# Optimization experiments

Measured on AMD Instinct MI355X. Metric: run time of the kernel, lower is better.

## Reference

```python
import jax, jax.numpy as jnp
import numpy as np

B, T, V, D, U, NT = 32, 512, 32000, 300, 300, 3


def setup_inputs() -> dict:
    key = jax.random.key(0)
    ks = jax.random.split(key, 10)
    s = 0.05
    return {
        "inputs": jax.random.randint(ks[0], (B, T), 0, V),
        "sequence_length": jax.random.randint(ks[1], (B,), 0, T),
        "emb": jax.random.normal(ks[2], (V, D), jnp.float32) * s,
        "Wk_f": jax.random.normal(ks[3], (D, 4 * U), jnp.float32) * s,
        "Wr_f": jax.random.normal(ks[4], (U, 4 * U), jnp.float32) * s,
        "b_f": jnp.zeros((4 * U,), jnp.float32),
        "Wk_b": jax.random.normal(ks[5], (D, 4 * U), jnp.float32) * s,
        "Wr_b": jax.random.normal(ks[6], (U, 4 * U), jnp.float32) * s,
        "b_b": jnp.zeros((4 * U,), jnp.float32),
        "fc_W": jax.random.normal(ks[7], (2 * U, NT), jnp.float32) * s,
        "fc_b": jnp.zeros((NT,), jnp.float32),
    }


def _lstm_scan(x, mask, Wk, Wr, b):
    # x: [B,T,D], mask: [B,T] bool. Keras semantics: masked steps carry h,c through.
    units = Wr.shape[0]
    zx = jnp.einsum('btd,dz->btz', x, Wk) + b        # precompute input projection
    zx_t = jnp.swapaxes(zx, 0, 1)                    # [T,B,4U]
    m_t = jnp.swapaxes(mask, 0, 1)                   # [T,B]

    def step(carry, inp):
        h, c = carry
        zxt, mt = inp
        z = zxt + h @ Wr                             # [B,4U]
        i, f, g, o = jnp.split(z, 4, axis=-1)
        c_new = jax.nn.sigmoid(f) * c + jax.nn.sigmoid(i) * jnp.tanh(g)
        h_new = jax.nn.sigmoid(o) * jnp.tanh(c_new)
        m = mt[:, None]
        h = jnp.where(m, h_new, h)
        c = jnp.where(m, c_new, c)
        return (h, c), h

    h0 = jnp.zeros((x.shape[0], units), x.dtype)
    _, hs = jax.lax.scan(step, (h0, h0), (zx_t, m_t))
    return jnp.swapaxes(hs, 0, 1)                    # [B,T,U]


def reference(inputs, sequence_length, emb, Wk_f, Wr_f, b_f, Wk_b, Wr_b, b_b, fc_W, fc_b):
    x = emb[inputs]                                   # [B,T,D]
    mask = jnp.arange(T)[None, :] < sequence_length[:, None]  # [B,T]
    h_fwd = _lstm_scan(x, mask, Wk_f, Wr_f, b_f)
    # backward direction: reverse time (input + mask), scan, reverse output back
    h_bwd = jnp.flip(_lstm_scan(jnp.flip(x, 1), jnp.flip(mask, 1), Wk_b, Wr_b, b_b), 1)
    h = jnp.concatenate([h_fwd, h_bwd], axis=-1)      # [B,T,2U]
    return h @ fc_W + fc_b                            # [B,T,NT]
```

## Files before the change

### kernel.cpp

```cpp
#include <hip/hip_runtime.h>
#include <stdint.h>


#define BB 32
#define TT 512
#define DD 300
#define UU 300
#define G4 1200
#define NTOK 3

#define KB   10
#define UPB  30
#define NCOL 120
#define KTILES 10
#define HSTR 320
#define HROW 304

#define WKROWS 1280
#define WKSTR  320

typedef uint16_t bf16_t;
typedef short  s16x8 __attribute__((ext_vector_type(8)));
typedef float  f32x4 __attribute__((ext_vector_type(4)));

union U8 { unsigned long long q[2]; s16x8 v; };

__device__ __forceinline__ float bf2f(uint16_t u) {
    union { uint32_t i; float f; } v; v.i = ((uint32_t)u) << 16; return v.f;
}
__device__ __forceinline__ uint16_t f2bf(float f) {
    union { uint32_t i; float f; } v; v.f = f;
    uint32_t r = v.i + 0x7fffu + ((v.i >> 16) & 1u);
    return (uint16_t)(r >> 16);
}
__device__ __forceinline__ float ldf(const void* base, size_t idx, int f32m) {
    return f32m ? ((const float*)base)[idx]
                : bf2f(((const uint16_t*)base)[idx]);
}

__device__ __forceinline__ f32x4 xpose4(f32x4 v, int lane) {
    f32x4 t, w, s, r;
    t[0] = __shfl_xor(v[0], 1); t[1] = __shfl_xor(v[1], 1);
    t[2] = __shfl_xor(v[2], 1); t[3] = __shfl_xor(v[3], 1);
    if ((lane & 1) == 0) { w[0]=v[0]; w[1]=t[0]; w[2]=v[2]; w[3]=t[2]; }
    else                 { w[0]=t[1]; w[1]=v[1]; w[2]=t[3]; w[3]=v[3]; }
    s[0] = __shfl_xor(w[0], 2); s[1] = __shfl_xor(w[1], 2);
    s[2] = __shfl_xor(w[2], 2); s[3] = __shfl_xor(w[3], 2);
    if ((lane & 2) == 0) { r[0]=w[0]; r[1]=w[1]; r[2]=s[0]; r[3]=s[1]; }
    else                 { r[0]=s[2]; r[1]=s[3]; r[2]=w[2]; r[3]=w[3]; }
    return r;
}

__device__ __forceinline__ float fsig(float x) {
    return __builtin_amdgcn_rcpf(1.f + __expf(-x));
}
__device__ __forceinline__ float ftanh(float x) {
    float cx = fminf(10.f, fmaxf(-10.f, x));
    float e = __expf(2.f * cx);
    return (e - 1.f) * __builtin_amdgcn_rcpf(e + 1.f);
}

__device__ __forceinline__ void gatefn(f32x4 zv, uint2 zp, bool m,
                                       float& c, float& h) {
    float zi = zv[0] + bf2f((uint16_t)(zp.x & 0xffff));
    float zf = zv[1] + bf2f((uint16_t)(zp.x >> 16));
    float zg = zv[2] + bf2f((uint16_t)(zp.y & 0xffff));
    float zo = zv[3] + bf2f((uint16_t)(zp.y >> 16));
    float si = fsig(zi);
    float sf = fsig(zf);
    float so = fsig(zo);
    float tg = ftanh(zg);
    float cn = sf * c + si * tg;
    float hn = so * ftanh(cn);
    if (m) { c = cn; h = hn; }
}

__global__ void detect_dtype(const uint16_t* __restrict__ emb_u16,
                             int* __restrict__ flag) {
    __shared__ float red[256];
    const int tid = threadIdx.x;
    float m = 0.f;
    for (int k = tid; k < 4096; k += 256)
        m = fmaxf(m, fabsf(bf2f(emb_u16[2 * k])));
    red[tid] = m;
    __syncthreads();
    for (int s = 128; s > 0; s >>= 1) {
        if (tid < s) red[tid] = fmaxf(red[tid], red[tid + s]);
        __syncthreads();
    }
    if (tid == 0) flag[0] = (red[0] > 1.0e3f) ? 1 : 0;
}

__global__ void prep_wrp(const void* __restrict__ Wr_f,
                         const void* __restrict__ Wr_b,
                         bf16_t* __restrict__ WrPT_f,
                         bf16_t* __restrict__ WrPT_b,
                         const int* __restrict__ flagp) {
    const int f32m = *flagp;
    int idx = blockIdx.x * 256 + threadIdx.x;
    const void* src = blockIdx.y ? Wr_b : Wr_f;
    bf16_t*     dst = blockIdx.y ? WrPT_b : WrPT_f;
    if (idx < G4 * HROW) {
        int p = idx / HROW;
        int k = idx - p * HROW;
        int u = p >> 2, g = p & 3;
        float v = (k < DD) ? ldf(src, (size_t)k * G4 + g * UU + u, f32m) : 0.f;
        dst[idx] = f2bf(v);
    }
}

__global__ void prep_wkt(const void* __restrict__ Wk_f, const void* __restrict__ b_f,
                         const void* __restrict__ Wk_b, const void* __restrict__ b_b,
                         bf16_t* __restrict__ WkT, bf16_t* __restrict__ biasP,
                         const int* __restrict__ flagp) {
    const int f32m = *flagp;
    const int dir = blockIdx.y;
    const void* Wk = dir ? Wk_b : Wk_f;
    const void* bs = dir ? b_b  : b_f;
    bf16_t* dst = WkT + (size_t)dir * (WKROWS * WKSTR);
    int idx = blockIdx.x * 256 + threadIdx.x;
    if (idx < WKROWS * WKSTR) {
        int p = idx / WKSTR;
        int k = idx - p * WKSTR;
        int u = p >> 2, g = p & 3;
        float v = (p < G4 && k < DD) ? ldf(Wk, (size_t)k * G4 + g * UU + u, f32m)
                                     : 0.f;
        dst[idx] = f2bf(v);
        if (idx < WKROWS) {
            int pp = idx, uu = pp >> 2, gg = pp & 3;
            biasP[dir * WKROWS + idx] =
                (pp < G4) ? f2bf(ldf(bs, gg * UU + uu, f32m)) : (bf16_t)0;
        }
    }
}

__global__ void init_state(bf16_t* __restrict__ Hglob, int* __restrict__ flags) {
    int i = blockIdx.x * 256 + threadIdx.x;
    if (i < 2 * 2 * BB * HROW) Hglob[i] = 0;
    if (i < 2 * TT * 16) flags[i] = 0;
}

#define ZM 64
#define ZN 128
__global__ __launch_bounds__(256, 2) void zx_gemm2(
    const int* __restrict__ inputs, const void* __restrict__ emb,
    const bf16_t* __restrict__ WkTall, const bf16_t* __restrict__ biasP,
    bf16_t* __restrict__ zxf, bf16_t* __restrict__ zxb,
    const int* __restrict__ flagp) {

    const int f32m = *flagp;
    const int dir = blockIdx.z;
    const bf16_t* WkT = WkTall + (size_t)dir * (WKROWS * WKSTR);
    const bf16_t* bp  = biasP + dir * WKROWS;
    bf16_t* out = dir ? zxb : zxf;

    const int tid = threadIdx.x;
    const int pb = blockIdx.x * ZN;
    const int rowBase = blockIdx.y * ZM;

    __shared__ __align__(16) uint16_t Alds[ZM * HSTR];
    __shared__ int rowids[ZM];

    if (tid < ZM) rowids[tid] = inputs[rowBase + tid];
    for (int i = tid; i < ZM * HSTR; i += 256) Alds[i] = 0;
    __syncthreads();

    for (int i = tid; i < ZM * 38; i += 256) {
        int r = i / 38, g = i - 38 * r;
        int k0 = g * 8;
        const size_t eb = (size_t)rowids[r] * DD + k0;
        uint16_t tmp[8];
        if (g < 37) {
            if (f32m) {
                const float* ef = (const float*)emb + eb;
#pragma unroll
                for (int e = 0; e < 8; e++) tmp[e] = f2bf(ef[e]);
            } else {
                *(uint4*)tmp = *(const uint4*)((const uint16_t*)emb + eb);
            }
        } else {
#pragma unroll
            for (int e = 0; e < 8; e++) {
                int k = k0 + e;
                tmp[e] = (k < DD)
                    ? (f32m ? f2bf(((const float*)emb)[(size_t)rowids[r] * DD + k])
                            : ((const uint16_t*)emb)[(size_t)rowids[r] * DD + k])
                    : (uint16_t)0;
            }
        }
        *(uint4*)&Alds[r * HSTR + ((g ^ (r & 7)) << 3)] = *(uint4*)tmp;
    }
    __syncthreads();

    const int lane = tid & 63;
    const int wv   = tid >> 6;
    const int q    = lane >> 4;
    const int c16  = lane & 15;
    const int n0   = 32 * wv;
    const int sw7  = c16 & 7;

    f32x4 acc[4][2];
#pragma unroll
    for (int mt = 0; mt < 4; mt++)
        for (int nh = 0; nh < 2; nh++) acc[mt][nh] = (f32x4){0.f,0.f,0.f,0.f};

    const int p0 = pb + n0 + c16;
    const int p1 = p0 + 16;
#pragma unroll
    for (int kt = 0; kt < KTILES; kt++) {
        int k0 = 32 * kt + 8 * q;
        int sw = (((kt * 4 + q) ^ sw7) << 3);
        s16x8 b0 = *(const s16x8*)&WkT[(size_t)p0 * WKSTR + k0];
        s16x8 b1 = *(const s16x8*)&WkT[(size_t)p1 * WKSTR + k0];
#pragma unroll
        for (int mt = 0; mt < 4; mt++) {
            s16x8 af = *(const s16x8*)&Alds[(16 * mt + c16) * HSTR + sw];
            acc[mt][0] = __builtin_amdgcn_mfma_f32_16x16x32_bf16(af, b0, acc[mt][0], 0, 0, 0);
            acc[mt][1] = __builtin_amdgcn_mfma_f32_16x16x32_bf16(af, b1, acc[mt][1], 0, 0, 0);
        }
    }

    __syncthreads();
    float* Cs = (float*)Alds;
#pragma unroll
    for (int mt = 0; mt < 4; mt++)
#pragma unroll
        for (int nh = 0; nh < 2; nh++)
#pragma unroll
            for (int r = 0; r < 4; r++)
                Cs[(16 * mt + 4 * q + r) * 132 + n0 + 16 * nh + c16] = acc[mt][nh][r];
    __syncthreads();

    for (int i = tid; i < ZM * (ZN / 2); i += 256) {
        int r = i >> 6, cc = (i & 63) * 2;
        int p = pb + cc;
        if (p < G4) {
            float v0 = Cs[r * 132 + cc]     + bf2f(bp[p]);
            float v1 = Cs[r * 132 + cc + 1] + bf2f(bp[p + 1]);
            uint32_t pk = (uint32_t)f2bf(v0) | ((uint32_t)f2bf(v1) << 16);
            *(uint32_t*)&out[(size_t)(rowBase + r) * G4 + p] = pk;
        }
    }
}

__global__ __launch_bounds__(256, 1) void lstm_rec4(
    const bf16_t* __restrict__ zxf, const bf16_t* __restrict__ zxb,
    const bf16_t* __restrict__ WrPT_f, const bf16_t* __restrict__ WrPT_b,
    const int* __restrict__ seqlen,
    bf16_t* __restrict__ Hglob, int* __restrict__ flags,
    bf16_t* __restrict__ hf, bf16_t* __restrict__ hb) {

    const int blk = blockIdx.x % KB;
    const int dir = blockIdx.x / KB;
    const bf16_t* zx   = dir ? zxb    : zxf;
    const bf16_t* WrPT = dir ? WrPT_b : WrPT_f;
    bf16_t*       hout = dir ? hb : hf;
    bf16_t*       Hg   = Hglob + (size_t)dir * (2 * BB * HROW);
    int*          fbase = flags + dir * (TT * 16);

    __shared__ __align__(16) uint16_t Hlds[BB * HSTR];
    __shared__ uint16_t hstage[BB * UPB];

    const int tid  = threadIdx.x;
    const int lane = tid & 63;
    const int wv   = tid >> 6;
    const int q    = lane >> 4;
    const int c16  = lane & 15;
    const int n0   = 32 * wv;
    const int sw7  = c16 & 7;
    const int k4   = c16 >> 2;
    const int j4   = c16 & 3;
    const int u0   = 8 * wv + k4;
    const int b0   = 4 * q + j4;
    const bool v1  = (u0 + 4 < UPB);
    const bool pollme = (lane < KB) && (lane != blk);

    for (int i = tid; i < BB * HSTR; i += 256) Hlds[i] = 0;
    U8 Bf0[KTILES], Bf1[KTILES];
#pragma unroll
    for (int kt = 0; kt < KTILES; kt++) {
        int k0 = 32 * kt + 8 * q;
        int col0 = n0 + c16, col1 = n0 + 16 + c16;
        U8 z; z.q[0] = 0; z.q[1] = 0;
        Bf0[kt] = z; Bf1[kt] = z;
        if (k0 < 304) {
            if (col0 < NCOL)
                Bf0[kt].v = *(const s16x8*)&WrPT[(size_t)(NCOL * blk + col0) * HROW + k0];
            if (col1 < NCOL)
                Bf1[kt].v = *(const s16x8*)&WrPT[(size_t)(NCOL * blk + col1) * HROW + k0];
        }
    }
    float c00 = 0.f, c01 = 0.f, c10 = 0.f, c11 = 0.f;
    float h00 = 0.f, h01 = 0.f, h10 = 0.f, h11 = 0.f;
    const int L0 = seqlen[b0];
    const int L1 = seqlen[b0 + 16];
    __syncthreads();

    for (int ts = 0; ts < TT; ts++) {
        const int t = dir ? (TT - 1 - ts) : ts;

        const size_t zr0 = ((size_t)(b0 * TT + t)) * G4 + NCOL * blk;
        const size_t zr1 = ((size_t)((b0 + 16) * TT + t)) * G4 + NCOL * blk;
        uint2 z00 = *(const uint2*)&zx[zr0 + 4 * u0];
        uint2 z10 = *(const uint2*)&zx[zr1 + 4 * u0];
        uint2 z01 = {0, 0}, z11 = {0, 0};
        if (v1) {
            z01 = *(const uint2*)&zx[zr0 + 4 * (u0 + 4)];
            z11 = *(const uint2*)&zx[zr1 + 4 * (u0 + 4)];
        }

        if (ts > 0) {
            int* fl = fbase + (ts - 1) * 16;
            int a = pollme ? __hip_atomic_load(&fl[lane], __ATOMIC_RELAXED,
                                               __HIP_MEMORY_SCOPE_AGENT) : 1;
            if (!__all(a != 0)) {
                int b = pollme ? __hip_atomic_load(&fl[lane], __ATOMIC_RELAXED,
                                                   __HIP_MEMORY_SCOPE_AGENT) : 1;
                int c = pollme ? __hip_atomic_load(&fl[lane], __ATOMIC_RELAXED,
                                                   __HIP_MEMORY_SCOPE_AGENT) : 1;
                for (;;) {
                    if (__all(a != 0)) break;
                    a = b; b = c;
                    c = pollme ? __hip_atomic_load(&fl[lane], __ATOMIC_RELAXED,
                                                   __HIP_MEMORY_SCOPE_AGENT) : 1;
                }
            }
        }

        const unsigned long long* Hsrc64 =
            (const unsigned long long*)(Hg + (size_t)(ts & 1) * (BB * HROW));
        unsigned long long hv[10];
#pragma unroll
        for (int k = 0; k < 9; k++)
            hv[k] = __hip_atomic_load(&Hsrc64[tid + 256 * k], __ATOMIC_RELAXED,
                                      __HIP_MEMORY_SCOPE_AGENT);
        if (tid < 128)
            hv[9] = __hip_atomic_load(&Hsrc64[2304 + tid], __ATOMIC_RELAXED,
                                      __HIP_MEMORY_SCOPE_AGENT);
#pragma unroll
        for (int k = 0; k < 9; k++) {
            int i = tid + 256 * k;
            int b = i / 76, x = i - 76 * b;
            *(unsigned long long*)
                &Hlds[b * HSTR + ((((x >> 1) ^ (b & 7)) << 3) | ((x & 1) << 2))]
                = hv[k];
        }
        if (tid < 128) {
            int i = 2304 + tid;
            int b = i / 76, x = i - 76 * b;
            *(unsigned long long*)
                &Hlds[b * HSTR + ((((x >> 1) ^ (b & 7)) << 3) | ((x & 1) << 2))]
                = hv[9];
        }
        __syncthreads();

        f32x4 acc00 = {0.f,0.f,0.f,0.f}, acc01 = {0.f,0.f,0.f,0.f};
        f32x4 acc10 = {0.f,0.f,0.f,0.f}, acc11 = {0.f,0.f,0.f,0.f};
#pragma unroll
        for (int kt = 0; kt < KTILES; kt++) {
            int sw = (((kt * 4 + q) ^ sw7) << 3);
            s16x8 a0 = *(const s16x8*)&Hlds[c16 * HSTR + sw];
            s16x8 a1 = *(const s16x8*)&Hlds[(c16 + 16) * HSTR + sw];
            acc00 = __builtin_amdgcn_mfma_f32_16x16x32_bf16(a0, Bf0[kt].v, acc00, 0, 0, 0);
            acc01 = __builtin_amdgcn_mfma_f32_16x16x32_bf16(a0, Bf1[kt].v, acc01, 0, 0, 0);
            acc10 = __builtin_amdgcn_mfma_f32_16x16x32_bf16(a1, Bf0[kt].v, acc10, 0, 0, 0);
            acc11 = __builtin_amdgcn_mfma_f32_16x16x32_bf16(a1, Bf1[kt].v, acc11, 0, 0, 0);
        }

        f32x4 t00 = xpose4(acc00, lane);
        f32x4 t01 = xpose4(acc01, lane);
        f32x4 t10 = xpose4(acc10, lane);
        f32x4 t11 = xpose4(acc11, lane);
        const bool m0 = (t < L0);
        const bool m1 = (t < L1);
        gatefn(t00, z00, m0, c00, h00);
        gatefn(t01, z01, m0, c01, h01);
        gatefn(t10, z10, m1, c10, h10);
        gatefn(t11, z11, m1, c11, h11);

        hstage[b0 * UPB + u0]        = f2bf(h00);
        hstage[(b0 + 16) * UPB + u0] = f2bf(h10);
        if (v1) {
            hstage[b0 * UPB + u0 + 4]        = f2bf(h01);
            hstage[(b0 + 16) * UPB + u0 + 4] = f2bf(h11);
        }
        __syncthreads();

        if (ts < TT - 1) {
            bf16_t* Hdst = Hg + (size_t)((ts + 1) & 1) * (BB * HROW);
            for (int i = tid; i < BB * (UPB / 2); i += 256) {
                int b = i / (UPB / 2), k = i - b * (UPB / 2);
                uint32_t val = (uint32_t)hstage[b * UPB + 2 * k] |
                               ((uint32_t)hstage[b * UPB + 2 * k + 1] << 16);
                __hip_atomic_store(
                    (uint32_t*)&Hdst[b * HROW + UPB * blk + 2 * k], val,
                    __ATOMIC_RELAXED, __HIP_MEMORY_SCOPE_AGENT);
            }
            __syncthreads();
            if (tid == 0)
                __hip_atomic_store(&fbase[ts * 16 + blk], 1, __ATOMIC_RELAXED,
                                   __HIP_MEMORY_SCOPE_AGENT);
        }

        for (int i = tid; i < BB * (UPB / 2); i += 256) {
            int b = i / (UPB / 2), k = i - b * (UPB / 2);
            uint32_t val = (uint32_t)hstage[b * UPB + 2 * k] |
                           ((uint32_t)hstage[b * UPB + 2 * k + 1] << 16);
            *(uint32_t*)&hout[((size_t)(b * TT + t)) * UU + UPB * blk + 2 * k] = val;
        }
    }
}

__global__ __launch_bounds__(256) void fc_out(
    const bf16_t* __restrict__ hf, const bf16_t* __restrict__ hb,
    const void* __restrict__ fcW, const void* __restrict__ fcb,
    void* __restrict__ out, const int* __restrict__ flagp) {

    const int f32m = *flagp;
    __shared__ float W[2 * UU * NTOK];
    __shared__ float bias[NTOK];
    const int tid = threadIdx.x;
    for (int i = tid; i < 2 * UU * NTOK; i += 256) W[i] = ldf(fcW, i, f32m);
    if (tid < NTOK) bias[tid] = ldf(fcb, tid, f32m);
    __syncthreads();

    const int r = blockIdx.x * 256 + tid;
    const bf16_t* hfr = hf + (size_t)r * UU;
    const bf16_t* hbr = hb + (size_t)r * UU;
    float s0 = bias[0], s1 = bias[1], s2 = bias[2];
    for (int u = 0; u < UU; u++) {
        float f = bf2f(hfr[u]);
        s0 += f * W[u * 3 + 0];
        s1 += f * W[u * 3 + 1];
        s2 += f * W[u * 3 + 2];
    }
    for (int u = 0; u < UU; u++) {
        float f = bf2f(hbr[u]);
        s0 += f * W[(UU + u) * 3 + 0];
        s1 += f * W[(UU + u) * 3 + 1];
        s2 += f * W[(UU + u) * 3 + 2];
    }
    if (f32m) {
        float* o = (float*)out;
        o[(size_t)r * 3 + 0] = s0;
        o[(size_t)r * 3 + 1] = s1;
        o[(size_t)r * 3 + 2] = s2;
    } else {
        bf16_t* o = (bf16_t*)out;
        o[(size_t)r * 3 + 0] = f2bf(s0);
        o[(size_t)r * 3 + 1] = f2bf(s1);
        o[(size_t)r * 3 + 2] = f2bf(s2);
    }
}

extern "C" void kernel_launch(void* const* d_in, const int* in_sizes, int n_in,
                              void* d_out, int out_size, void* d_ws, size_t ws_size,
                              hipStream_t stream) {
    const int* inputs = (const int*)d_in[0];
    const int* seqlen = (const int*)d_in[1];
    const void* emb  = d_in[2];
    const void* Wk_f = d_in[3];
    const void* Wr_f = d_in[4];
    const void* b_f  = d_in[5];
    const void* Wk_b = d_in[6];
    const void* Wr_b = d_in[7];
    const void* b_b  = d_in[8];
    const void* fcW  = d_in[9];
    const void* fcb  = d_in[10];

    char* ws = (char*)d_ws;
    int*    flag   = (int*)(ws + 0);
    int*    flags  = (int*)(ws + 64);
    bf16_t* Hglob  = (bf16_t*)(ws + 65664);
    bf16_t* WrPT_f = (bf16_t*)(ws + 143488);
    bf16_t* WrPT_b = (bf16_t*)(ws + 873088);
    bf16_t* zxPf   = (bf16_t*)(ws + 1602688);
    bf16_t* zxPb   = (bf16_t*)(ws + 40924288);
    bf16_t* hfbuf  = (bf16_t*)(ws + 80245888);
    bf16_t* hbbuf  = (bf16_t*)(ws + 90076288);
    bf16_t* WkT    = hfbuf;
    bf16_t* biasP  = hfbuf + 2 * WKROWS * WKSTR;

    detect_dtype<<<1, 256, 0, stream>>>((const uint16_t*)emb, flag);
    {
        dim3 grid((G4 * HROW + 255) / 256, 2);
        prep_wrp<<<grid, 256, 0, stream>>>(Wr_f, Wr_b, WrPT_f, WrPT_b, flag);
    }
    {
        dim3 grid((WKROWS * WKSTR + 255) / 256, 2);
        prep_wkt<<<grid, 256, 0, stream>>>(Wk_f, b_f, Wk_b, b_b, WkT, biasP, flag);
    }
    init_state<<<64, 256, 0, stream>>>(Hglob, flags);
    {
        dim3 grid(10, 256, 2);
        zx_gemm2<<<grid, 256, 0, stream>>>(inputs, emb, WkT, biasP,
                                           zxPf, zxPb, flag);
    }
    lstm_rec4<<<2 * KB, 256, 0, stream>>>(zxPf, zxPb, WrPT_f, WrPT_b, seqlen,
                                          Hglob, flags, hfbuf, hbbuf);
    fc_out<<<(BB * TT) / 256, 256, 0, stream>>>(hfbuf, hbbuf, fcW, fcb,
                                                d_out, flag);
}
```

Before: 1.823 ms.

## Loop over all output column tiles per block to reuse gathered embedding rows

The input-projection GEMM now has each block gather its 64 embedding rows into LDS once and then iterate over all 10 column tiles, instead of launching 10 blocks that each re-gather the same rows. The epilogue drops the LDS staging and writes bf16 pairs straight from registers, using a lane shuffle to pack adjacent columns. This cuts redundant embedding gathers, zero-fills and barriers, but leaves only 512 blocks, fewer than before, and the direct stores are less coalesced.

```diff
diff --git a/kernel.cpp b/kernel.cpp
--- a/kernel.cpp
+++ b/kernel.cpp
@@ -142,21 +142,20 @@
 
 #define ZM 64
 #define ZN 128
-__global__ __launch_bounds__(256, 2) void zx_gemm2(
+__global__ __launch_bounds__(256, 2) void zx_gemm3(
     const int* __restrict__ inputs, const void* __restrict__ emb,
     const bf16_t* __restrict__ WkTall, const bf16_t* __restrict__ biasP,
     bf16_t* __restrict__ zxf, bf16_t* __restrict__ zxb,
     const int* __restrict__ flagp) {
 
     const int f32m = *flagp;
-    const int dir = blockIdx.z;
+    const int dir = blockIdx.y;
     const bf16_t* WkT = WkTall + (size_t)dir * (WKROWS * WKSTR);
     const bf16_t* bp  = biasP + dir * WKROWS;
     bf16_t* out = dir ? zxb : zxf;
 
     const int tid = threadIdx.x;
-    const int pb = blockIdx.x * ZN;
-    const int rowBase = blockIdx.y * ZM;
+    const int rowBase = blockIdx.x * ZM;
 
     __shared__ __align__(16) uint16_t Alds[ZM * HSTR];
     __shared__ int rowids[ZM];
@@ -198,47 +197,51 @@
     const int c16  = lane & 15;
     const int n0   = 32 * wv;
     const int sw7  = c16 & 7;
-
-    f32x4 acc[4][2];
-#pragma unroll
-    for (int mt = 0; mt < 4; mt++)
-        for (int nh = 0; nh < 2; nh++) acc[mt][nh] = (f32x4){0.f,0.f,0.f,0.f};
-
-    const int p0 = pb + n0 + c16;
-    const int p1 = p0 + 16;
-#pragma unroll
-    for (int kt = 0; kt < KTILES; kt++) {
-        int k0 = 32 * kt + 8 * q;
-        int sw = (((kt * 4 + q) ^ sw7) << 3);
-        s16x8 b0 = *(const s16x8*)&WkT[(size_t)p0 * WKSTR + k0];
-        s16x8 b1 = *(const s16x8*)&WkT[(size_t)p1 * WKSTR + k0];
+    const bool evn = ((lane & 1) == 0);
+
+    for (int nt = 0; nt < 10; nt++) {
+        const int pb = nt * ZN;
+        const int p0 = pb + n0 + c16;
+        const int p1 = p0 + 16;
+        const float bv0 = bf2f(bp[p0]);
+        const float bv1 = bf2f(bp[p1]);
+
+        f32x4 acc[4][2];
+#pragma unroll
+        for (int mt = 0; mt < 4; mt++)
+            for (int nh = 0; nh < 2; nh++) acc[mt][nh] = (f32x4){0.f,0.f,0.f,0.f};
+
+#pragma unroll
+        for (int kt = 0; kt < KTILES; kt++) {
+            int k0 = 32 * kt + 8 * q;
+            int sw = (((kt * 4 + q) ^ sw7) << 3);
+            s16x8 b0 = *(const s16x8*)&WkT[(size_t)p0 * WKSTR + k0];
+            s16x8 b1 = *(const s16x8*)&WkT[(size_t)p1 * WKSTR + k0];
+#pragma unroll
+            for (int mt = 0; mt < 4; mt++) {
+                s16x8 af = *(const s16x8*)&Alds[(16 * mt + c16) * HSTR + sw];
+                acc[mt][0] = __builtin_amdgcn_mfma_f32_16x16x32_bf16(af, b0, acc[mt][0], 0, 0, 0);
+                acc[mt][1] = __builtin_amdgcn_mfma_f32_16x16x32_bf16(af, b1, acc[mt][1], 0, 0, 0);
+            }
+        }
+
 #pragma unroll
         for (int mt = 0; mt < 4; mt++) {
-            s16x8 af = *(const s16x8*)&Alds[(16 * mt + c16) * HSTR + sw];
-            acc[mt][0] = __builtin_amdgcn_mfma_f32_16x16x32_bf16(af, b0, acc[mt][0], 0, 0, 0);
-            acc[mt][1] = __builtin_amdgcn_mfma_f32_16x16x32_bf16(af, b1, acc[mt][1], 0, 0, 0);
-        }
-    }
-
-    __syncthreads();
-    float* Cs = (float*)Alds;
-#pragma unroll
-    for (int mt = 0; mt < 4; mt++)
-#pragma unroll
-        for (int nh = 0; nh < 2; nh++)
-#pragma unroll
-            for (int r = 0; r < 4; r++)
-                Cs[(16 * mt + 4 * q + r) * 132 + n0 + 16 * nh + c16] = acc[mt][nh][r];
-    __syncthreads();
-
-    for (int i = tid; i < ZM * (ZN / 2); i += 256) {
-        int r = i >> 6, cc = (i & 63) * 2;
-        int p = pb + cc;
-        if (p < G4) {
-            float v0 = Cs[r * 132 + cc]     + bf2f(bp[p]);
-            float v1 = Cs[r * 132 + cc + 1] + bf2f(bp[p + 1]);
-            uint32_t pk = (uint32_t)f2bf(v0) | ((uint32_t)f2bf(v1) << 16);
-            *(uint32_t*)&out[(size_t)(rowBase + r) * G4 + p] = pk;
+#pragma unroll
+            for (int nh = 0; nh < 2; nh++) {
+                const int p = (nh == 0) ? p0 : p1;
+                const float bv = (nh == 0) ? bv0 : bv1;
+#pragma unroll
+                for (int r = 0; r < 4; r++) {
+                    uint32_t mine = f2bf(acc[mt][nh][r] + bv);
+                    uint32_t other = (uint32_t)__shfl_xor((int)mine, 1);
+                    if (evn && p < G4) {
+                        uint32_t pk = mine | (other << 16);
+                        int row = rowBase + 16 * mt + 4 * q + r;
+                        *(uint32_t*)&out[(size_t)row * G4 + p] = pk;
+                    }
+                }
+            }
         }
     }
 }
@@ -492,8 +495,8 @@
     }
     init_state<<<64, 256, 0, stream>>>(Hglob, flags);
     {
-        dim3 grid(10, 256, 2);
-        zx_gemm2<<<grid, 256, 0, stream>>>(inputs, emb, WkT, biasP,
+        dim3 grid(256, 2);
+        zx_gemm3<<<grid, 256, 0, stream>>>(inputs, emb, WkT, biasP,
                                            zxPf, zxPb, flag);
     }
     lstm_rec4<<<2 * KB, 256, 0, stream>>>(zxPf, zxPb, WrPT_f, WrPT_b, seqlen,
```

Measured after the change: 1.723 ms. 1.06x faster.
